# Kernel tuning notes

Hardware: AMD Instinct MI355X
Metric: run time of the kernel (lower is better)

## Reference

```python
import jax, jax.numpy as jnp
import numpy as np

N = 50000      # nodes
E = 640000     # edges
F_IN = 64      # node feature dim
H = 128        # hidden channels
G = 256        # graphs in batch
NEG_SLOPE = 0.2
BN_EPS = 1e-5


def setup_inputs() -> dict:
    key = jax.random.key(0)
    ks = jax.random.split(key, 32)
    rn = lambda k, shape, s=0.1: jax.random.normal(k, shape, dtype=jnp.float32) * s
    inp = {
        'x': jax.random.normal(ks[0], (N, F_IN), dtype=jnp.float32),
        'edge_index': jax.random.randint(ks[1], (2, E), 0, N, dtype=jnp.int32),
        'batch': jnp.sort(jax.random.randint(ks[2], (N,), 0, G, dtype=jnp.int32)),
        # GATConv 1
        'W1': rn(ks[3], (F_IN, H)), 'as1': rn(ks[4], (H,)), 'ad1': rn(ks[5], (H,)), 'b1': jnp.zeros((H,), jnp.float32),
        # GATConv 2
        'W2': rn(ks[6], (H, H)), 'as2': rn(ks[7], (H,)), 'ad2': rn(ks[8], (H,)), 'b2': jnp.zeros((H,), jnp.float32),
        # GATConv 3
        'W3': rn(ks[9], (H, H)), 'as3': rn(ks[10], (H,)), 'ad3': rn(ks[11], (H,)), 'b3': jnp.zeros((H,), jnp.float32),
        # BatchNorm (inference: running stats)
        'g1': jnp.ones((H,), jnp.float32), 'be1': jnp.zeros((H,), jnp.float32), 'm1': rn(ks[12], (H,), 0.01), 'v1': jnp.ones((H,), jnp.float32),
        'g2': jnp.ones((H,), jnp.float32), 'be2': jnp.zeros((H,), jnp.float32), 'm2': rn(ks[13], (H,), 0.01), 'v2': jnp.ones((H,), jnp.float32),
        'g3': jnp.ones((H,), jnp.float32), 'be3': jnp.zeros((H,), jnp.float32), 'm3': rn(ks[14], (H,), 0.01), 'v3': jnp.ones((H,), jnp.float32),
        # MLP head
        'lw1': rn(ks[15], (H, H)), 'lb1': jnp.zeros((H,), jnp.float32),
        'lw2': rn(ks[16], (H, 1)), 'lb2': jnp.zeros((1,), jnp.float32),
    }
    return inp


def gat_layer(x, src, dst, W, a_src, a_dst, b, n):
    # PyG GATConv, heads=1: linear, per-edge attention, segment softmax over dst, scatter-add.
    h = x @ W                                  # [N, H]
    s_src = h @ a_src                          # [N]
    s_dst = h @ a_dst                          # [N]
    e = jax.nn.leaky_relu(s_src[src] + s_dst[dst], NEG_SLOPE)   # [E']
    m = jax.ops.segment_max(e, dst, num_segments=n)
    ex = jnp.exp(e - m[dst])
    denom = jax.ops.segment_sum(ex, dst, num_segments=n)
    coef = ex / denom[dst]                     # softmax per destination node
    out = jax.ops.segment_sum(coef[:, None] * h[src], dst, num_segments=n)
    return out + b


def batch_norm(x, g, b, mean, var):
    return (x - mean) * jax.lax.rsqrt(var + BN_EPS) * g + b


def reference(x, edge_index, batch,
              W1, as1, ad1, b1, W2, as2, ad2, b2, W3, as3, ad3, b3,
              g1, be1, m1, v1, g2, be2, m2, v2, g3, be3, m3, v3,
              lw1, lb1, lw2, lb2):
    n = x.shape[0]
    loops = jnp.arange(n, dtype=edge_index.dtype)      # PyG adds self-loops by default
    src = jnp.concatenate([edge_index[0], loops])
    dst = jnp.concatenate([edge_index[1], loops])

    h = gat_layer(x, src, dst, W1, as1, ad1, b1, n)
    h = jax.nn.relu(batch_norm(h, g1, be1, m1, v1))
    h = gat_layer(h, src, dst, W2, as2, ad2, b2, n)
    h = jax.nn.relu(batch_norm(h, g2, be2, m2, v2))
    h = gat_layer(h, src, dst, W3, as3, ad3, b3, n)
    h = jax.nn.relu(batch_norm(h, g3, be3, m3, v3))

    # global_mean_pool
    counts = jax.ops.segment_sum(jnp.ones((n,), h.dtype), batch, num_segments=G)
    pooled = jax.ops.segment_sum(h, batch, num_segments=G) / jnp.maximum(counts, 1.0)[:, None]

    out = jax.nn.relu(pooled @ lw1 + lb1)
    out = out @ lw2 + lb2                               # [G, 1]
    return out
```

## Files before the change

kernel.cpp:

```cpp
#include <hip/hip_runtime.h>

#define HD 128
#define NEG 0.2f
#define BNEPS 1e-5f

typedef unsigned int uint32;
typedef __attribute__((ext_vector_type(8))) short short8;
typedef __attribute__((ext_vector_type(4))) float floatx4;


__device__ inline float wave_sum_f(float v) {
#pragma unroll
  for (int off = 32; off; off >>= 1) v += __shfl_xor(v, off, 64);
  return v;
}
__device__ inline int wave_iscan_i(int v, int lane) {
#pragma unroll
  for (int off = 1; off < 64; off <<= 1) {
    int t = __shfl_up(v, off, 64);
    if (lane >= off) v += t;
  }
  return v;
}
__device__ inline uint32 f2bf(float f) {
  uint32 u = __float_as_uint(f);
  return (u + 0x7fffu + ((u >> 16) & 1u)) >> 16;
}
__device__ inline void kpair(int kc, int lg, int e2, bool perm, int& k_lo, int& k_hi) {
  if (!perm) {
    k_lo = kc * 32 + lg * 8 + e2 * 2;
    k_hi = k_lo + 1;
  } else {
    int w = kc * 16 + lg * 4 + e2;
    k_lo = ((w >> 4) << 5) + (w & 15);
    k_hi = k_lo + 16;
  }
}

__global__ __launch_bounds__(256)
void k_pack(const float* __restrict__ W1, const float* __restrict__ as1v,
            const float* __restrict__ ad1v, const float* __restrict__ W2,
            const float* __restrict__ as2v, const float* __restrict__ ad2v,
            const float* __restrict__ W3, const float* __restrict__ as3v,
            const float* __restrict__ ad3v, uint32* __restrict__ PW1,
            uint32* __restrict__ PW2, uint32* __restrict__ PW3,
            uint32* __restrict__ BFA1, uint32* __restrict__ BFA2,
            uint32* __restrict__ BFA3, int* __restrict__ deg,
            int* __restrict__ gcnt, int n) {
  const int b = blockIdx.x, t = threadIdx.x;
  if (b >= 83) {
    const int i = (b - 83) * 256 + t;
    if (i < n) deg[i] = 0;
    if (b == 83 && t == 0) gcnt[0] = 0;
    return;
  }
  if (b < 80) {
    const float* W;
    uint32* PW;
    int KC, local;
    bool perm;
    if (b < 16) { W = W1; PW = PW1; KC = 2; perm = false; local = b; }
    else if (b < 48) { W = W2; PW = PW2; KC = 4; perm = true; local = b - 16; }
    else { W = W3; PW = PW3; KC = 4; perm = true; local = b - 48; }
    const int idx = local * 256 + t;
    const int e2 = idx & 3, l = (idx >> 2) & 63, f = idx >> 8;
    const int kc = f % KC, ct = f / KC;
    int k_lo, k_hi;
    kpair(kc, l >> 4, e2, perm, k_lo, k_hi);
    const int col = ct * 16 + (l & 15);
    PW[idx] = f2bf(W[k_lo * HD + col]) | (f2bf(W[k_hi * HD + col]) << 16);
  } else {
    const int layer = b - 80;
    const float* W = layer == 0 ? W1 : layer == 1 ? W2 : W3;
    const float* av = layer == 0 ? as1v : layer == 1 ? as2v : as3v;
    const float* dv = layer == 0 ? ad1v : layer == 1 ? ad2v : ad3v;
    uint32* BFA = layer == 0 ? BFA1 : layer == 1 ? BFA2 : BFA3;
    const int K = layer == 0 ? 64 : 128, KC = K / 32;
    const bool perm = layer != 0;
    __shared__ float ws[128], wd[128];
    if (t < K) {
      float s = 0.f, d = 0.f;
      for (int j = 0; j < HD; ++j) {
        const float w = W[t * HD + j];
        s = fmaf(w, av[j], s);
        d = fmaf(w, dv[j], d);
      }
      ws[t] = s;
      wd[t] = d;
    }
    __syncthreads();
    const int total = KC * 256;
    for (int idx = t; idx < total; idx += 256) {
      const int e2 = idx & 3, l = (idx >> 2) & 63, kc = idx >> 8;
      int k_lo, k_hi;
      kpair(kc, l >> 4, e2, perm, k_lo, k_hi);
      const int li = l & 15;
      const float lo = li == 0 ? ws[k_lo] : li == 1 ? wd[k_lo] : 0.f;
      const float hi = li == 0 ? ws[k_hi] : li == 1 ? wd[k_hi] : 0.f;
      BFA[idx] = f2bf(lo) | (f2bf(hi) << 16);
    }
  }
}

__global__ __launch_bounds__(256)
void k_alloc(const int* __restrict__ deg, int* __restrict__ gcnt,
             int2* __restrict__ offs2, int* __restrict__ csr,
             int* __restrict__ cursor, int n) {
  const int t = threadIdx.x, lane = t & 63, wave = t >> 6;
  const int i = blockIdx.x * 256 + t;
  const int v = (i < n) ? deg[i] + 1 : 0;
  const int x = wave_iscan_i(v, lane);
  __shared__ int wsum[4];
  __shared__ int bbase;
  if (lane == 63) wsum[wave] = x;
  __syncthreads();
  if (t == 0) bbase = atomicAdd(gcnt, wsum[0] + wsum[1] + wsum[2] + wsum[3]);
  __syncthreads();
  int add = bbase;
#pragma unroll
  for (int w = 0; w < 4; ++w)
    if (w < wave) add += wsum[w];
  const int start = add + x - v;
  if (i < n) {
    offs2[i] = make_int2(start, start + v);
    csr[start] = i;
    cursor[i] = start + 1;
  }
}

__global__ void k_fill_edges(const int* __restrict__ src, const int* __restrict__ dst,
                             int* __restrict__ cursor, int* __restrict__ csr, int E) {
  int i = blockIdx.x * blockDim.x + threadIdx.x;
  if (i < E) { int p = atomicAdd(&cursor[dst[i]], 1); csr[p] = src[i]; }
}

template <int K, bool BF16IN>
__device__ inline void gemm_body(int bid, const void* __restrict__ Xv,
                                 const uint32* __restrict__ PW,
                                 const uint32* __restrict__ BFA,
                                 uint32* __restrict__ Hh, float* __restrict__ ssrc,
                                 float* __restrict__ sdst, int n) {
  constexpr int KC = K / 32;
  __shared__ uint32 Xl[64 * K / 2];
  const int t = threadIdx.x;
  const int wv = t >> 6, l = t & 63;
  const int rowbase = bid * 64;

  short8 bfr[2][KC];
#pragma unroll
  for (int c2 = 0; c2 < 2; ++c2)
#pragma unroll
    for (int kc = 0; kc < KC; ++kc)
      bfr[c2][kc] = *((const short8*)PW + ((wv * 2 + c2) * KC + kc) * 64 + l);
  short8 bfa[KC];
  if (wv == 0) {
#pragma unroll
    for (int kc = 0; kc < KC; ++kc) bfa[kc] = *((const short8*)BFA + kc * 64 + l);
  }

  if (BF16IN) {
    const uint32* Xb = (const uint32*)Xv;
#pragma unroll
    for (int B = t; B < 64 * (K / 8); B += 256) {
      const int row = B / (K / 8), cb = B % (K / 8);
      const int r = min(rowbase + row, n - 1);
      const uint4 v = *(const uint4*)&Xb[(long)r * (K / 2) + cb * 4];
      *(uint4*)&Xl[row * (K / 2) + (cb ^ (row & 7)) * 4] = v;
    }
  } else {
    const float* X = (const float*)Xv;
    for (int i = t; i < 64 * (K / 4); i += 256) {
      const int row = i / (K / 4), kq = i % (K / 4);
      const int r = min(rowbase + row, n - 1);
      const float4 v = *(const float4*)&X[(long)r * K + kq * 4];
      uint2 p;
      p.x = f2bf(v.x) | (f2bf(v.y) << 16);
      p.y = f2bf(v.z) | (f2bf(v.w) << 16);
      int byte = row * (K * 2) + kq * 8;
      byte ^= (row & 7) << 4;
      *(uint2*)((char*)Xl + byte) = p;
    }
  }
  __syncthreads();

  floatx4 acc[4][2], acc2[4];
#pragma unroll
  for (int rt = 0; rt < 4; ++rt) {
    acc[rt][0] = (floatx4){0.f, 0.f, 0.f, 0.f};
    acc[rt][1] = (floatx4){0.f, 0.f, 0.f, 0.f};
    acc2[rt] = (floatx4){0.f, 0.f, 0.f, 0.f};
  }
  const int row_l = l & 15, kgrp = l >> 4;
#pragma unroll
  for (int rt = 0; rt < 4; ++rt) {
    const int row = rt * 16 + row_l;
#pragma unroll
    for (int kc = 0; kc < KC; ++kc) {
      const int byte = (row * (K * 2) + kc * 64 + kgrp * 16) ^ ((row & 7) << 4);
      const short8 af = *(const short8*)((const char*)Xl + byte);
      acc[rt][0] = __builtin_amdgcn_mfma_f32_16x16x32_bf16(af, bfr[0][kc], acc[rt][0], 0, 0, 0);
      acc[rt][1] = __builtin_amdgcn_mfma_f32_16x16x32_bf16(af, bfr[1][kc], acc[rt][1], 0, 0, 0);
      if (wv == 0)
        acc2[rt] = __builtin_amdgcn_mfma_f32_16x16x32_bf16(af, bfa[kc], acc2[rt], 0, 0, 0);
    }
  }

#pragma unroll
  for (int rt = 0; rt < 4; ++rt) {
#pragma unroll
    for (int r = 0; r < 4; ++r) {
      const int R = rowbase + rt * 16 + kgrp * 4 + r;
      if (R < n)
        Hh[(long)R * 64 + wv * 16 + row_l] =
            f2bf(acc[rt][0][r]) | (f2bf(acc[rt][1][r]) << 16);
    }
  }
  if (wv == 0 && row_l < 2) {
    float* tgt = (row_l == 0) ? ssrc : sdst;
#pragma unroll
    for (int rt = 0; rt < 4; ++rt)
#pragma unroll
      for (int r = 0; r < 4; ++r) {
        const int R = rowbase + rt * 16 + kgrp * 4 + r;
        if (R < n) tgt[R] = acc2[rt][r];
      }
  }
}

__global__ __launch_bounds__(256)
void k_gemm1_hist(const void* __restrict__ Xv, const uint32* __restrict__ PW,
                  const uint32* __restrict__ BFA, uint32* __restrict__ Hh,
                  float* __restrict__ ssrc, float* __restrict__ sdst, int n,
                  const int* __restrict__ dst, int* __restrict__ deg, int E, int GB) {
  const int b = blockIdx.x;
  if (b < GB) {
    gemm_body<64, false>(b, Xv, PW, BFA, Hh, ssrc, sdst, n);
  } else {
    const int i = (b - GB) * 256 + threadIdx.x;
    if (i < E) atomicAdd(&deg[dst[i]], 1);
  }
}

template <int K>
__global__ __launch_bounds__(256)
void k_gemm_mfma(const void* __restrict__ Xv, const uint32* __restrict__ PW,
                 const uint32* __restrict__ BFA, uint32* __restrict__ Hh,
                 float* __restrict__ ssrc, float* __restrict__ sdst, int n) {
  gemm_body<K, true>(blockIdx.x, Xv, PW, BFA, Hh, ssrc, sdst, n);
}

__global__ __launch_bounds__(256)
void k_agg(const uint32* __restrict__ Hh, const float* __restrict__ ssrc,
           const float* __restrict__ sdst, const int2* __restrict__ offs2,
           const int* __restrict__ csr, const float* __restrict__ bias,
           const float* __restrict__ gam, const float* __restrict__ bet,
           const float* __restrict__ mu, const float* __restrict__ var,
           uint32* __restrict__ Ybf, int n) {
  const int wid = (blockIdx.x * blockDim.x + threadIdx.x) >> 6;
  const int lane = threadIdx.x & 63;
  if (wid >= n) return;
  const int2 se = offs2[wid];
  const float sdv = sdst[wid];
  const int c0 = (lane >> 4) * 32 + (lane & 15);
  const int c1 = c0 + 16;
  float acc0 = 0.f, acc1 = 0.f, denom = 0.f;
  for (int base = se.x; base < se.y; base += 64) {
    const int m = min(64, se.y - base);
    int sidx = 0;
    float p = 0.f;
    if (lane < m) {
      sidx = csr[base + lane];
      const float tt = ssrc[sidx] + sdv;
      const float e = (tt > 0.f) ? tt : NEG * tt;
      p = __expf(e);
    }
    denom += wave_sum_f(p);
    const uint32 pu = __float_as_uint(p);
    for (int jj = 0; jj < m; jj += 16) {
      uint32 g[16];
#pragma unroll
      for (int u = 0; u < 16; ++u) {
        if (jj + u < m) {
          const int s = __builtin_amdgcn_readlane(sidx, jj + u);
          g[u] = Hh[(long)s * 64 + lane];
        }
      }
#pragma unroll
      for (int u = 0; u < 16; ++u) {
        if (jj + u < m) {
          const float w = __uint_as_float(__builtin_amdgcn_readlane(pu, jj + u));
          acc0 = fmaf(w, __uint_as_float(g[u] << 16), acc0);
          acc1 = fmaf(w, __uint_as_float(g[u] & 0xffff0000u), acc1);
        }
      }
    }
  }
  const float inv = 1.f / denom;
  float v0 = acc0 * inv + bias[c0];
  float v1 = acc1 * inv + bias[c1];
  const float sc0 = gam[c0] * rsqrtf(var[c0] + BNEPS);
  const float sc1 = gam[c1] * rsqrtf(var[c1] + BNEPS);
  v0 = fmaxf((v0 - mu[c0]) * sc0 + bet[c0], 0.f);
  v1 = fmaxf((v1 - mu[c1]) * sc1 + bet[c1], 0.f);
  Ybf[(long)wid * 64 + lane] = f2bf(v0) | (f2bf(v1) << 16);
}

__global__ __launch_bounds__(256)
void k_pool_head(const uint32* __restrict__ Ybf, const int* __restrict__ batch, int n,
                 const float* __restrict__ lw1, const float* __restrict__ lb1,
                 const float* __restrict__ lw2, const float* __restrict__ lb2,
                 float* __restrict__ out) {
  const int g = blockIdx.x;
  const int wave = threadIdx.x >> 6, lane = threadIdx.x & 63;
  int lo = 0, hi = n;
  while (lo < hi) { int mid = (lo + hi) >> 1; if (batch[mid] < g) lo = mid + 1; else hi = mid; }
  const int start = lo;
  hi = n;
  while (lo < hi) { int mid = (lo + hi) >> 1; if (batch[mid] < g + 1) lo = mid + 1; else hi = mid; }
  const int end = lo;
  const int c0 = (lane >> 4) * 32 + (lane & 15);
  const int c1 = c0 + 16;
  float m0 = 0.f, m1 = 0.f;
  for (int i = start + wave; i < end; i += 4) {
    const uint32 gv = Ybf[(long)i * 64 + lane];
    m0 += __uint_as_float(gv << 16);
    m1 += __uint_as_float(gv & 0xffff0000u);
  }
  __shared__ float red[4][HD];
  red[wave][c0] = m0;
  red[wave][c1] = m1;
  __syncthreads();
  if (wave == 0) {
    m0 = red[0][c0] + red[1][c0] + red[2][c0] + red[3][c0];
    m1 = red[0][c1] + red[1][c1] + red[2][c1] + red[3][c1];
    const float cnt = (float)(end - start);
    const float invc = (cnt > 0.f) ? 1.f / cnt : 0.f;
    m0 *= invc;
    m1 *= invc;
    float t0 = lb1[c0], t1 = lb1[c1];
    for (int k = 0; k < HD; ++k) {
      const int srcl = ((k >> 5) << 4) + (k & 15);
      const float pv = __shfl(((k >> 4) & 1) ? m1 : m0, srcl, 64);
      t0 = fmaf(pv, lw1[k * HD + c0], t0);
      t1 = fmaf(pv, lw1[k * HD + c1], t1);
    }
    t0 = fmaxf(t0, 0.f);
    t1 = fmaxf(t1, 0.f);
    float p = t0 * lw2[c0] + t1 * lw2[c1];
#pragma unroll
    for (int off = 32; off; off >>= 1) p += __shfl_xor(p, off, 64);
    if (lane == 0) out[g] = p + lb2[0];
  }
}


extern "C" void kernel_launch(void* const* d_in, const int* in_sizes, int n_in,
                              void* d_out, int out_size, void* d_ws, size_t ws_size,
                              hipStream_t stream) {
  const float* x = (const float*)d_in[0];
  const int* ei = (const int*)d_in[1];
  const int* batch = (const int*)d_in[2];
  const float* W1 = (const float*)d_in[3];
  const float* as1 = (const float*)d_in[4];
  const float* ad1 = (const float*)d_in[5];
  const float* b1 = (const float*)d_in[6];
  const float* W2 = (const float*)d_in[7];
  const float* as2 = (const float*)d_in[8];
  const float* ad2 = (const float*)d_in[9];
  const float* b2 = (const float*)d_in[10];
  const float* W3 = (const float*)d_in[11];
  const float* as3 = (const float*)d_in[12];
  const float* ad3 = (const float*)d_in[13];
  const float* b3 = (const float*)d_in[14];
  const float* g1 = (const float*)d_in[15];
  const float* be1 = (const float*)d_in[16];
  const float* m1 = (const float*)d_in[17];
  const float* v1 = (const float*)d_in[18];
  const float* g2 = (const float*)d_in[19];
  const float* be2 = (const float*)d_in[20];
  const float* m2 = (const float*)d_in[21];
  const float* v2 = (const float*)d_in[22];
  const float* g3 = (const float*)d_in[23];
  const float* be3 = (const float*)d_in[24];
  const float* m3 = (const float*)d_in[25];
  const float* v3 = (const float*)d_in[26];
  const float* lw1 = (const float*)d_in[27];
  const float* lb1 = (const float*)d_in[28];
  const float* lw2 = (const float*)d_in[29];
  const float* lb2 = (const float*)d_in[30];

  const int n = in_sizes[0] / 64;
  const int E = in_sizes[1] / 2;
  const int* src = ei;
  const int* dst = ei + E;

  uint32* hbuf = (uint32*)d_ws;
  uint32* ybuf = hbuf + (long)n * 64;
  float* ssrc = (float*)(ybuf + (long)n * 64);
  float* sdstv = ssrc + n;
  int* deg = (int*)(sdstv + n);
  int2* offs2 = (int2*)(deg + n);
  int* cursor = (int*)(offs2 + n);
  int* csr = cursor + n;
  int* gcnt = csr + (E + n);
  uint32* PW1 = (uint32*)(gcnt + 4);
  uint32* PW2 = PW1 + 4096;
  uint32* PW3 = PW2 + 8192;
  uint32* BFA1 = PW3 + 8192;
  uint32* BFA2 = BFA1 + 512;
  uint32* BFA3 = BFA2 + 1024;

  const int B = 256;
  dim3 blk(B);
  const int nb = (n + B - 1) / B;
  const int eb = (E + B - 1) / B;
  const int GB = (n + 63) / 64;

  k_pack<<<dim3(83 + nb), blk, 0, stream>>>(W1, as1, ad1, W2, as2, ad2, W3, as3, ad3,
                                            PW1, PW2, PW3, BFA1, BFA2, BFA3,
                                            deg, gcnt, n);
  k_gemm1_hist<<<dim3(GB + eb), blk, 0, stream>>>(x, PW1, BFA1, hbuf, ssrc, sdstv, n,
                                                  dst, deg, E, GB);
  k_alloc<<<dim3(nb), blk, 0, stream>>>(deg, gcnt, offs2, csr, cursor, n);
  k_fill_edges<<<dim3(eb), blk, 0, stream>>>(src, dst, cursor, csr, E);

  const dim3 agrid((n + 3) / 4);
  k_agg<<<agrid, blk, 0, stream>>>(hbuf, ssrc, sdstv, offs2, csr, b1, g1, be1, m1, v1, ybuf, n);
  k_gemm_mfma<128><<<dim3(GB), blk, 0, stream>>>(ybuf, PW2, BFA2, hbuf, ssrc, sdstv, n);
  k_agg<<<agrid, blk, 0, stream>>>(hbuf, ssrc, sdstv, offs2, csr, b2, g2, be2, m2, v2, ybuf, n);
  k_gemm_mfma<128><<<dim3(GB), blk, 0, stream>>>(ybuf, PW3, BFA3, hbuf, ssrc, sdstv, n);
  k_agg<<<agrid, blk, 0, stream>>>(hbuf, ssrc, sdstv, offs2, csr, b3, g3, be3, m3, v3, ybuf, n);
  k_pool_head<<<dim3(256), blk, 0, stream>>>(ybuf, batch, n, lw1, lb1, lw2, lb2,
                                             (float*)d_out);
}
```

Before: 235.1 us.

## Bucket CSR neighbors by source range and precompute folded BatchNorm affine

The degree histogram and fill cursors are split into 32 slots per destination node, keyed by source index high bits. Each node's CSR neighbor list therefore comes out roughly sorted by source range, which should improve locality of the feature gathers in the aggregation kernels. Bias and BatchNorm are also folded into one per-channel scale/shift float4 table computed once in the pack kernel, so each aggregation epilogue does a single fma. The cost is a 32x larger degree and cursor array to zero, scan and read, which adds memory traffic in the setup kernels.

```diff
diff --git a/kernel.cpp b/kernel.cpp
--- a/kernel.cpp
+++ b/kernel.cpp
@@ -3,6 +3,8 @@
 #define HD 128
 #define NEG 0.2f
 #define BNEPS 1e-5f
+#define BSH 11
+#define NBSLOT 32
 
 typedef unsigned int uint32;
 typedef __attribute__((ext_vector_type(8))) short short8;
@@ -42,15 +44,25 @@
             const float* __restrict__ ad1v, const float* __restrict__ W2,
             const float* __restrict__ as2v, const float* __restrict__ ad2v,
             const float* __restrict__ W3, const float* __restrict__ as3v,
-            const float* __restrict__ ad3v, uint32* __restrict__ PW1,
-            uint32* __restrict__ PW2, uint32* __restrict__ PW3,
-            uint32* __restrict__ BFA1, uint32* __restrict__ BFA2,
-            uint32* __restrict__ BFA3, int* __restrict__ deg,
-            int* __restrict__ gcnt, int n) {
+            const float* __restrict__ ad3v,
+            const float* __restrict__ b1, const float* __restrict__ g1,
+            const float* __restrict__ be1, const float* __restrict__ m1,
+            const float* __restrict__ v1,
+            const float* __restrict__ b2, const float* __restrict__ g2,
+            const float* __restrict__ be2, const float* __restrict__ m2,
+            const float* __restrict__ v2,
+            const float* __restrict__ b3, const float* __restrict__ g3,
+            const float* __restrict__ be3, const float* __restrict__ m3,
+            const float* __restrict__ v3,
+            uint32* __restrict__ PW1, uint32* __restrict__ PW2,
+            uint32* __restrict__ PW3, uint32* __restrict__ BFA1,
+            uint32* __restrict__ BFA2, uint32* __restrict__ BFA3,
+            float4* __restrict__ BNAB,
+            int* __restrict__ deg32, int* __restrict__ gcnt, int n) {
   const int b = blockIdx.x, t = threadIdx.x;
   if (b >= 83) {
     const int i = (b - 83) * 256 + t;
-    if (i < n) deg[i] = 0;
+    if (i < n * NBSLOT) deg32[i] = 0;
     if (b == 83 && t == 0) gcnt[0] = 0;
     return;
   }
@@ -74,6 +86,11 @@
     const float* W = layer == 0 ? W1 : layer == 1 ? W2 : W3;
     const float* av = layer == 0 ? as1v : layer == 1 ? as2v : as3v;
     const float* dv = layer == 0 ? ad1v : layer == 1 ? ad2v : ad3v;
+    const float* bb = layer == 0 ? b1 : layer == 1 ? b2 : b3;
+    const float* gg = layer == 0 ? g1 : layer == 1 ? g2 : g3;
+    const float* bt = layer == 0 ? be1 : layer == 1 ? be2 : be3;
+    const float* mm = layer == 0 ? m1 : layer == 1 ? m2 : m3;
+    const float* vv = layer == 0 ? v1 : layer == 1 ? v2 : v3;
     uint32* BFA = layer == 0 ? BFA1 : layer == 1 ? BFA2 : BFA3;
     const int K = layer == 0 ? 64 : 128, KC = K / 32;
     const bool perm = layer != 0;
@@ -99,17 +116,39 @@
       const float hi = li == 0 ? ws[k_hi] : li == 1 ? wd[k_hi] : 0.f;
       BFA[idx] = f2bf(lo) | (f2bf(hi) << 16);
     }
-  }
-}
-
-__global__ __launch_bounds__(256)
-void k_alloc(const int* __restrict__ deg, int* __restrict__ gcnt,
+    if (t < 64) {
+      const int c0 = (t >> 4) * 32 + (t & 15);
+      const int c1 = c0 + 16;
+      const float A0 = gg[c0] * rsqrtf(vv[c0] + BNEPS);
+      const float A1 = gg[c1] * rsqrtf(vv[c1] + BNEPS);
+      float4 r;
+      r.x = A0;
+      r.y = (bb[c0] - mm[c0]) * A0 + bt[c0];
+      r.z = A1;
+      r.w = (bb[c1] - mm[c1]) * A1 + bt[c1];
+      BNAB[layer * 64 + t] = r;
+    }
+  }
+}
+
+__global__ __launch_bounds__(256)
+void k_alloc(const int4* __restrict__ deg4, int* __restrict__ gcnt,
              int2* __restrict__ offs2, int* __restrict__ csr,
-             int* __restrict__ cursor, int n) {
+             int4* __restrict__ cursor4, int n) {
   const int t = threadIdx.x, lane = t & 63, wave = t >> 6;
   const int i = blockIdx.x * 256 + t;
-  const int v = (i < n) ? deg[i] + 1 : 0;
-  const int x = wave_iscan_i(v, lane);
+  int4 q[8];
+  int tot = 1;
+  if (i < n) {
+#pragma unroll
+    for (int u = 0; u < 8; ++u) {
+      q[u] = deg4[i * 8 + u];
+      tot += q[u].x + q[u].y + q[u].z + q[u].w;
+    }
+  } else {
+    tot = 0;
+  }
+  const int x = wave_iscan_i(tot, lane);
   __shared__ int wsum[4];
   __shared__ int bbase;
   if (lane == 63) wsum[wave] = x;
@@ -120,18 +159,31 @@
 #pragma unroll
   for (int w = 0; w < 4; ++w)
     if (w < wave) add += wsum[w];
-  const int start = add + x - v;
+  const int start = add + x - tot;
   if (i < n) {
-    offs2[i] = make_int2(start, start + v);
     csr[start] = i;
-    cursor[i] = start + 1;
+    int r = start + 1;
+#pragma unroll
+    for (int u = 0; u < 8; ++u) {
+      int4 c;
+      c.x = r; r += q[u].x;
+      c.y = r; r += q[u].y;
+      c.z = r; r += q[u].z;
+      c.w = r; r += q[u].w;
+      cursor4[i * 8 + u] = c;
+    }
+    offs2[i] = make_int2(start, r);
   }
 }
 
 __global__ void k_fill_edges(const int* __restrict__ src, const int* __restrict__ dst,
                              int* __restrict__ cursor, int* __restrict__ csr, int E) {
   int i = blockIdx.x * blockDim.x + threadIdx.x;
-  if (i < E) { int p = atomicAdd(&cursor[dst[i]], 1); csr[p] = src[i]; }
+  if (i < E) {
+    const int s = src[i];
+    const int p = atomicAdd(&cursor[dst[i] * NBSLOT + (s >> BSH)], 1);
+    csr[p] = s;
+  }
 }
 
 template <int K, bool BF16IN>
@@ -231,13 +283,14 @@
 void k_gemm1_hist(const void* __restrict__ Xv, const uint32* __restrict__ PW,
                   const uint32* __restrict__ BFA, uint32* __restrict__ Hh,
                   float* __restrict__ ssrc, float* __restrict__ sdst, int n,
-                  const int* __restrict__ dst, int* __restrict__ deg, int E, int GB) {
+                  const int* __restrict__ src, const int* __restrict__ dst,
+                  int* __restrict__ deg32, int E, int GB) {
   const int b = blockIdx.x;
   if (b < GB) {
     gemm_body<64, false>(b, Xv, PW, BFA, Hh, ssrc, sdst, n);
   } else {
     const int i = (b - GB) * 256 + threadIdx.x;
-    if (i < E) atomicAdd(&deg[dst[i]], 1);
+    if (i < E) atomicAdd(&deg32[dst[i] * NBSLOT + (src[i] >> BSH)], 1);
   }
 }
 
@@ -252,17 +305,13 @@
 __global__ __launch_bounds__(256)
 void k_agg(const uint32* __restrict__ Hh, const float* __restrict__ ssrc,
            const float* __restrict__ sdst, const int2* __restrict__ offs2,
-           const int* __restrict__ csr, const float* __restrict__ bias,
-           const float* __restrict__ gam, const float* __restrict__ bet,
-           const float* __restrict__ mu, const float* __restrict__ var,
+           const int* __restrict__ csr, const float4* __restrict__ BNAB,
            uint32* __restrict__ Ybf, int n) {
   const int wid = (blockIdx.x * blockDim.x + threadIdx.x) >> 6;
   const int lane = threadIdx.x & 63;
   if (wid >= n) return;
   const int2 se = offs2[wid];
   const float sdv = sdst[wid];
-  const int c0 = (lane >> 4) * 32 + (lane & 15);
-  const int c1 = c0 + 16;
   float acc0 = 0.f, acc1 = 0.f, denom = 0.f;
   for (int base = se.x; base < se.y; base += 64) {
     const int m = min(64, se.y - base);
@@ -296,12 +345,9 @@
     }
   }
   const float inv = 1.f / denom;
-  float v0 = acc0 * inv + bias[c0];
-  float v1 = acc1 * inv + bias[c1];
-  const float sc0 = gam[c0] * rsqrtf(var[c0] + BNEPS);
-  const float sc1 = gam[c1] * rsqrtf(var[c1] + BNEPS);
-  v0 = fmaxf((v0 - mu[c0]) * sc0 + bet[c0], 0.f);
-  v1 = fmaxf((v1 - mu[c1]) * sc1 + bet[c1], 0.f);
+  const float4 ab = BNAB[lane];
+  const float v0 = fmaxf(fmaf(acc0 * inv, ab.x, ab.y), 0.f);
+  const float v1 = fmaxf(fmaf(acc1 * inv, ab.z, ab.w), 0.f);
   Ybf[(long)wid * 64 + lane] = f2bf(v0) | (f2bf(v1) << 16);
 }
 
@@ -398,10 +444,10 @@
   uint32* ybuf = hbuf + (long)n * 64;
   float* ssrc = (float*)(ybuf + (long)n * 64);
   float* sdstv = ssrc + n;
-  int* deg = (int*)(sdstv + n);
-  int2* offs2 = (int2*)(deg + n);
+  int* deg32 = (int*)(sdstv + n);
+  int2* offs2 = (int2*)(deg32 + (long)n * NBSLOT);
   int* cursor = (int*)(offs2 + n);
-  int* csr = cursor + n;
+  int* csr = cursor + (long)n * NBSLOT;
   int* gcnt = csr + (E + n);
   uint32* PW1 = (uint32*)(gcnt + 4);
   uint32* PW2 = PW1 + 4096;
@@ -409,27 +455,31 @@
   uint32* BFA1 = PW3 + 8192;
   uint32* BFA2 = BFA1 + 512;
   uint32* BFA3 = BFA2 + 1024;
+  float4* BNAB = (float4*)(BFA3 + 1024);
 
   const int B = 256;
   dim3 blk(B);
   const int nb = (n + B - 1) / B;
   const int eb = (E + B - 1) / B;
+  const int zb = ((n * NBSLOT) + B - 1) / B;
   const int GB = (n + 63) / 64;
 
-  k_pack<<<dim3(83 + nb), blk, 0, stream>>>(W1, as1, ad1, W2, as2, ad2, W3, as3, ad3,
-                                            PW1, PW2, PW3, BFA1, BFA2, BFA3,
-                                            deg, gcnt, n);
+  k_pack<<<dim3(83 + zb), blk, 0, stream>>>(
+      W1, as1, ad1, W2, as2, ad2, W3, as3, ad3,
+      b1, g1, be1, m1, v1, b2, g2, be2, m2, v2, b3, g3, be3, m3, v3,
+      PW1, PW2, PW3, BFA1, BFA2, BFA3, BNAB, deg32, gcnt, n);
   k_gemm1_hist<<<dim3(GB + eb), blk, 0, stream>>>(x, PW1, BFA1, hbuf, ssrc, sdstv, n,
-                                                  dst, deg, E, GB);
-  k_alloc<<<dim3(nb), blk, 0, stream>>>(deg, gcnt, offs2, csr, cursor, n);
+                                                  src, dst, deg32, E, GB);
+  k_alloc<<<dim3(nb), blk, 0, stream>>>((const int4*)deg32, gcnt, offs2, csr,
+                                        (int4*)cursor, n);
   k_fill_edges<<<dim3(eb), blk, 0, stream>>>(src, dst, cursor, csr, E);
 
   const dim3 agrid((n + 3) / 4);
-  k_agg<<<agrid, blk, 0, stream>>>(hbuf, ssrc, sdstv, offs2, csr, b1, g1, be1, m1, v1, ybuf, n);
+  k_agg<<<agrid, blk, 0, stream>>>(hbuf, ssrc, sdstv, offs2, csr, BNAB + 0, ybuf, n);
   k_gemm_mfma<128><<<dim3(GB), blk, 0, stream>>>(ybuf, PW2, BFA2, hbuf, ssrc, sdstv, n);
-  k_agg<<<agrid, blk, 0, stream>>>(hbuf, ssrc, sdstv, offs2, csr, b2, g2, be2, m2, v2, ybuf, n);
+  k_agg<<<agrid, blk, 0, stream>>>(hbuf, ssrc, sdstv, offs2, csr, BNAB + 64, ybuf, n);
   k_gemm_mfma<128><<<dim3(GB), blk, 0, stream>>>(ybuf, PW3, BFA3, hbuf, ssrc, sdstv, n);
-  k_agg<<<agrid, blk, 0, stream>>>(hbuf, ssrc, sdstv, offs2, csr, b3, g3, be3, m3, v3, ybuf, n);
+  k_agg<<<agrid, blk, 0, stream>>>(hbuf, ssrc, sdstv, offs2, csr, BNAB + 128, ybuf, n);
   k_pool_head<<<dim3(256), blk, 0, stream>>>(ybuf, batch, n, lw1, lb1, lw2, lb2,
                                              (float*)d_out);
 }
```

After: 229.3 us. 1.03x faster.
